# Kernel optimization log

Hardware: AMD Instinct MI355X
Metric: run time of the kernel (lower is better)

The kernel has to match this reference:

```python
import jax, jax.numpy as jnp
import numpy as np
from jax import lax

SIGMAS = [0.5, 1.0, 2.0, 4.0, 8.0]
FILTER_SIZE = int(4 * SIGMAS[-1] + 1)  # 33
PAD = int(2 * SIGMAS[-1])              # 16
DR = 1.0
C1 = (0.01 * DR) ** 2
C2 = (0.03 * DR) ** 2
ALPHA = 0.025
COMPENSATION = 200.0
LAMBDA_PIXEL = 100.0


def _gauss_2d(size, sigma):
    coords = np.arange(size, dtype=np.float32) - size // 2
    g = np.exp(-coords ** 2 / (2.0 * sigma ** 2))
    g = g / g.sum()
    return np.outer(g, g)  # (size, size)


def _build_g_masks():
    # Shape (15, 1, 33, 33): 3 identical copies per sigma, interleaved as in torch code.
    m = np.zeros((3 * len(SIGMAS), 1, FILTER_SIZE, FILTER_SIZE), dtype=np.float32)
    for idx, s in enumerate(SIGMAS):
        k = _gauss_2d(FILTER_SIZE, s)
        m[3 * idx + 0, 0] = k
        m[3 * idx + 1, 0] = k
        m[3 * idx + 2, 0] = k
    return jnp.asarray(m)


def _gconv(t, w):
    # Grouped conv, groups=3 (torch semantics: out channel j in group j // (O/3),
    # group g reads input channel g). 'same' padding via explicit PAD.
    return lax.conv_general_dilated(
        t, w, window_strides=(1, 1), padding=[(PAD, PAD), (PAD, PAD)],
        feature_group_count=3, dimension_numbers=('NCHW', 'OIHW', 'NCHW'))


def setup_inputs() -> dict:
    key = jax.random.key(0)
    k1, k2, k3 = jax.random.split(key, 3)
    x = jax.random.normal(k1, (8, 3, 512, 512), dtype=jnp.float32)
    y = jax.random.normal(k2, (8, 3, 512, 512), dtype=jnp.float32)
    disc_out = jax.random.normal(k3, (8, 1, 62, 62), dtype=jnp.float32)
    return {"x": x, "y": y, "disc_out": disc_out, "g_masks": _build_g_masks()}


def reference(x, y, disc_out, g_masks):
    # denormalize: tanh output [-1,1] -> [0,1]
    x = x * 0.5 + 0.5
    y = y * 0.5 + 0.5

    mux = _gconv(x, g_masks)          # (B, 15, H, W)
    muy = _gconv(y, g_masks)
    mux2 = mux * mux
    muy2 = muy * muy
    muxy = mux * muy
    sigmax2 = _gconv(x * x, g_masks) - mux2
    sigmay2 = _gconv(y * y, g_masks) - muy2
    sigmaxy = _gconv(x * y, g_masks) - muxy

    l = (2.0 * muxy + C1) / (mux2 + muy2 + C1)
    cs = (2.0 * sigmaxy + C2) / (sigmax2 + sigmay2 + C2)

    lM = l[:, -1] * l[:, -2] * l[:, -3]       # (B, H, W)
    PIcs = jnp.prod(cs, axis=1)               # (B, H, W)
    loss_ms_ssim = 1.0 - lM * PIcs

    loss_l1 = jnp.abs(x - y)                  # (B, 3, H, W)
    # narrow(0, -3, 3) -> last 3 filters (sigma=8), grouped conv then channel mean
    gaussian_l1 = _gconv(loss_l1, g_masks[-3:]).mean(axis=1)  # (B, H, W)

    loss_mix = ALPHA * loss_ms_ssim + (1.0 - ALPHA) * gaussian_l1 / DR
    loss_mix = COMPENSATION * loss_mix

    # GeneratorLoss: lambda_pixel * L1(x, y) + MSE(disc_out, 1)
    gen_loss = LAMBDA_PIXEL * jnp.mean(jnp.abs(x - y)) + jnp.mean((disc_out - 1.0) ** 2)

    return (loss_mix.mean() + gen_loss) / 2.0
```

## Files before the change

### kernel.cpp

```cpp
#include <hip/hip_runtime.h>
#include <stdint.h>


#define TILE 32
#define HALO 16
#define SSTR 72
#define PTPLN (32 * SSTR)
#define NT   256

#define C1c 1.0e-4f
#define C2c 9.0e-4f

typedef short bf16x8 __attribute__((ext_vector_type(8)));
typedef float f32x4  __attribute__((ext_vector_type(4)));
typedef unsigned short ush;

constexpr double cexp(double xx) {
  if (xx < -700.0) return 0.0;
  const double ln2 = 0.6931471805599453, il2 = 1.4426950408889634;
  double kd = xx * il2;
  long long k = (long long)(kd + (kd >= 0 ? 0.5 : -0.5));
  double r = xx - (double)k * ln2;
  double t = 1.0, s = 1.0;
  for (int i = 1; i <= 22; ++i) { t *= r / (double)i; s += t; }
  double p = 1.0, base = (k >= 0) ? 2.0 : 0.5;
  long long n = (k >= 0) ? k : -k;
  while (n) { if (n & 1) p *= base; base *= base; n >>= 1; }
  return s * p;
}
constexpr float gsi(double sigma) {
  double inv = 1.0 / (2.0 * sigma * sigma);
  double s = 0.0;
  for (int k = -16; k <= 16; ++k) s += cexp(-(double)(k * k) * inv);
  return (float)(1.0 / s);
}
constexpr float SI05 = gsi(0.5), SI10 = gsi(1.0), SI20 = gsi(2.0),
                SI40 = gsi(4.0), SI80 = gsi(8.0);

__device__ __forceinline__ unsigned f2bf_pk(float lo, float hi) {
  union { float f; unsigned u; } a, b; a.f = lo; b.f = hi;
  return __builtin_amdgcn_perm(b.u + 0x8000u, a.u + 0x8000u, 0x07060302u);
}
__device__ __forceinline__ ush f2bf1(float f) {
  union { float f; unsigned u; } c; c.f = f;
  return (ush)((c.u + 0x8000u) >> 16);
}

struct WFrag {
  bf16x8 h[2][2];
};

template<int SIG>
__device__ __forceinline__ void build_wm(ush* __restrict__ WM,
                                         const float (*__restrict__ wf5)[40],
                                         int tid, int wave, int lane,
                                         WFrag& W) {
  __syncthreads();
  #pragma unroll
  for (int i = 0; i < 8; ++i) {
    const int idx = i * 256 + tid;
    const int m = idx >> 6, k = idx & 63;
    const int t = k - m;
    const int tc = t < 0 ? 0 : (t > 32 ? 32 : t);
    float v = wf5[SIG][tc];
    v = (t >= 0 && t <= 32) ? v : 0.f;
    WM[m * SSTR + k] = f2bf1(v);
  }
  __syncthreads();
  const int l16 = lane & 15, quad = lane >> 4;
  #pragma unroll
  for (int t = 0; t < 2; ++t)
    #pragma unroll
    for (int c = 0; c < 2; ++c)
      W.h[t][c] = *(const bf16x8*)(WM + (t * 16 + l16) * SSTR + quad * 8 + 32 * c);
}

template<int NQ>
__device__ __forceinline__ void conv_pass(const bf16x8 (&A)[NQ][2],
                                          const WFrag& W,
                                          ush* __restrict__ PT,
                                          int wave, int lane, f32x4* V) {
  const int l16 = lane & 15, quad = lane >> 4;
  const int m0 = wave * 16;
  #pragma unroll
  for (int q = 0; q < NQ; ++q) {
    #pragma unroll
    for (int nt = 0; nt < 2; ++nt) {
      f32x4 acc = {0.f, 0.f, 0.f, 0.f};
      acc = __builtin_amdgcn_mfma_f32_16x16x32_bf16(A[q][0], W.h[nt][0], acc, 0, 0, 0);
      acc = __builtin_amdgcn_mfma_f32_16x16x32_bf16(A[q][1], W.h[nt][1], acc, 0, 0, 0);
      uint2 u;
      u.x = f2bf_pk(acc[0], acc[1]);
      u.y = f2bf_pk(acc[2], acc[3]);
      *(uint2*)(PT + q * PTPLN + (nt * 16 + l16) * SSTR + m0 + quad * 4) = u;
    }
  }
  const bf16x8 wv0 = (wave & 2) ? W.h[1][0] : W.h[0][0];
  const bf16x8 wv1 = (wave & 2) ? W.h[1][1] : W.h[0][1];
  __syncthreads();
  const int n0 = (wave & 1) * 16;
  #pragma unroll
  for (int q = 0; q < NQ; ++q) {
    const ush* pp = PT + q * PTPLN + (n0 + l16) * SSTR + quad * 8;
    const bf16x8 b0 = *(const bf16x8*)pp;
    const bf16x8 b1 = *(const bf16x8*)(pp + 32);
    f32x4 acc = {0.f, 0.f, 0.f, 0.f};
    acc = __builtin_amdgcn_mfma_f32_16x16x32_bf16(wv0, b0, acc, 0, 0, 0);
    acc = __builtin_amdgcn_mfma_f32_16x16x32_bf16(wv1, b1, acc, 0, 0, 0);
    V[q] = acc;
  }
}

__device__ __forceinline__ void ssim_fold(const f32x4* V, int mult, bool last,
                                          float* PIcs) {
  #pragma unroll
  for (int r = 0; r < 4; ++r) {
    const float mux = V[0][r], muy = V[1][r];
    const float A = mux * muy;
    const float Bq = mux * mux + muy * muy;
    const float S = V[2][r] + V[3][r] - Bq;
    const float sxy = V[4][r] - A;
    const float cs = (2.f * sxy + C2c) * __builtin_amdgcn_rcpf(S + C2c);
    float p = cs;
    if (mult >= 2) p *= cs;
    if (mult >= 3) p *= cs;
    if (last) {
      const float l = (2.f * A + C1c) * __builtin_amdgcn_rcpf(Bq + C1c);
      p *= l * l * l;
    }
    PIcs[r] *= p;
  }
}

__global__ __launch_bounds__(NT)
void msssim_fused_kernel(const float* __restrict__ x, const float* __restrict__ y,
                         const float* __restrict__ disc,
                         float* __restrict__ partials) {
  __shared__ ush PT[5 * PTPLN];
  __shared__ ush WM[32 * SSTR];
  __shared__ float wf5[5][40];
  __shared__ float red[12];

  const int tid = threadIdx.x;
  const int wave = tid >> 6, lane = tid & 63;
  const int l16 = lane & 15, quad = lane >> 4;
  const int bx = blockIdx.x, by = blockIdx.y, b = blockIdx.z;
  const int x0 = bx * TILE - HALO, y0 = by * TILE - HALO;
  const int blk = (b * 16 + by) * 16 + bx;

  const int gy = y0 + wave * 16 + l16;
  const int cbase = x0 + quad * 8;
  const bool rowok = (gy >= 0) && (gy < 512);

  float d2 = 0.f;
  { const int di = blk * 16 + tid;
    if (tid < 16 && di < 8 * 62 * 62) { const float dd = disc[di] - 1.f; d2 = dd * dd; } }

  if (tid < 165) {
    const int sig = tid / 33;
    const int k = tid - sig * 33;
    const float d = (float)(k - 16);
    float inv, si;
    if (sig == 0)      { inv = 2.0f;       si = SI05; }
    else if (sig == 1) { inv = 0.5f;       si = SI10; }
    else if (sig == 2) { inv = 0.125f;     si = SI20; }
    else if (sig == 3) { inv = 0.03125f;   si = SI40; }
    else               { inv = 0.0078125f; si = SI80; }
    wf5[sig][k] = __expf(-d * d * inv) * si;
  }

  float xr[16], yr[16];
  auto frag_loads = [&](int ch) {
    const float* __restrict__ xs = x + (size_t)(b * 3 + ch) * 262144;
    const float* __restrict__ ys = y + (size_t)(b * 3 + ch) * 262144;
    #pragma unroll
    for (int c = 0; c < 2; ++c) {
      const int g0 = cbase + 32 * c;
      if (rowok && g0 >= 0 && g0 <= 504) {
        const float* px = xs + gy * 512 + g0;
        const float* py = ys + gy * 512 + g0;
        const float4 a0 = *(const float4*)px;
        const float4 a1 = *(const float4*)(px + 4);
        const float4 b0 = *(const float4*)py;
        const float4 b1 = *(const float4*)(py + 4);
        xr[c*8+0]=a0.x; xr[c*8+1]=a0.y; xr[c*8+2]=a0.z; xr[c*8+3]=a0.w;
        xr[c*8+4]=a1.x; xr[c*8+5]=a1.y; xr[c*8+6]=a1.z; xr[c*8+7]=a1.w;
        yr[c*8+0]=b0.x; yr[c*8+1]=b0.y; yr[c*8+2]=b0.z; yr[c*8+3]=b0.w;
        yr[c*8+4]=b1.x; yr[c*8+5]=b1.y; yr[c*8+6]=b1.z; yr[c*8+7]=b1.w;
      } else {
        #pragma unroll
        for (int e = 0; e < 8; ++e) {
          const int g = g0 + e;
          const bool ok = rowok && (g >= 0) && (g < 512);
          xr[c*8+e] = ok ? xs[gy * 512 + g] : 0.f;
          yr[c*8+e] = ok ? ys[gy * 512 + g] : 0.f;
        }
      }
    }
  };

  float PIcs[4] = {1.f, 1.f, 1.f, 1.f};
  float sadf[16];
  #pragma unroll
  for (int e = 0; e < 16; ++e) sadf[e] = 0.f;

  f32x4 V[5];
  WFrag W;
  bf16x8 AF[5][2];

  auto derive = [&]() {
    #pragma unroll
    for (int c = 0; c < 2; ++c) {
      float xf[8], yf[8];
      #pragma unroll
      for (int e = 0; e < 8; ++e) {
        xf[e] = fmaf(xr[c*8+e], 0.5f, 0.5f);
        yf[e] = fmaf(yr[c*8+e], 0.5f, 0.5f);
        sadf[c*8+e] += fabsf(xf[e] - yf[e]);
      }
      union { unsigned u[4]; bf16x8 v; } w0, w1, w2, w3, w4;
      #pragma unroll
      for (int p = 0; p < 4; ++p) {
        w0.u[p] = f2bf_pk(xf[2*p],           xf[2*p+1]);
        w1.u[p] = f2bf_pk(yf[2*p],           yf[2*p+1]);
        w2.u[p] = f2bf_pk(xf[2*p]*xf[2*p],   xf[2*p+1]*xf[2*p+1]);
        w3.u[p] = f2bf_pk(yf[2*p]*yf[2*p],   yf[2*p+1]*yf[2*p+1]);
        w4.u[p] = f2bf_pk(xf[2*p]*yf[2*p],   xf[2*p+1]*yf[2*p+1]);
      }
      AF[0][c] = w0.v; AF[1][c] = w1.v; AF[2][c] = w2.v;
      AF[3][c] = w3.v; AF[4][c] = w4.v;
    }
  };

  frag_loads(0);
  derive();
  frag_loads(1);
  build_wm<0>(WM, wf5, tid, wave, lane, W);
  conv_pass<5>(AF, W, PT, wave, lane, V);
  ssim_fold(V, 3, false, PIcs);
  build_wm<1>(WM, wf5, tid, wave, lane, W);
  conv_pass<5>(AF, W, PT, wave, lane, V);
  ssim_fold(V, 2, false, PIcs);

  derive();
  frag_loads(2);
  __syncthreads();
  conv_pass<5>(AF, W, PT, wave, lane, V);
  ssim_fold(V, 1, false, PIcs);
  build_wm<2>(WM, wf5, tid, wave, lane, W);
  conv_pass<5>(AF, W, PT, wave, lane, V);
  ssim_fold(V, 3, false, PIcs);
  build_wm<3>(WM, wf5, tid, wave, lane, W);
  conv_pass<5>(AF, W, PT, wave, lane, V);
  ssim_fold(V, 1, false, PIcs);

  derive();
  __syncthreads();
  conv_pass<5>(AF, W, PT, wave, lane, V);
  ssim_fold(V, 2, false, PIcs);
  build_wm<4>(WM, wf5, tid, wave, lane, W);
  conv_pass<5>(AF, W, PT, wave, lane, V);
  ssim_fold(V, 3, true, PIcs);

  bf16x8 SF[1][2];
  #pragma unroll
  for (int c = 0; c < 2; ++c) {
    union { unsigned u[4]; bf16x8 v; } w;
    #pragma unroll
    for (int p = 0; p < 4; ++p)
      w.u[p] = f2bf_pk(sadf[c*8+2*p], sadf[c*8+2*p+1]);
    SF[0][c] = w.v;
  }
  __syncthreads();
  f32x4 V1[1];
  conv_pass<1>(SF, W, PT, wave, lane, V1);

  float absacc = 0.f;
  if (wave == 1 || wave == 2) {
    if (quad >= 2) {
      #pragma unroll
      for (int e = 0; e < 8; ++e) absacc += sadf[e];
    } else {
      #pragma unroll
      for (int e = 0; e < 8; ++e) absacc += sadf[8 + e];
    }
  }

  float mixsum = 0.f;
  #pragma unroll
  for (int r = 0; r < 4; ++r) {
    const float ssim = 1.f - PIcs[r];
    mixsum += 200.f * (0.025f * ssim + 0.975f * (V1[0][r] * (1.f / 3.f)));
  }

  #pragma unroll
  for (int off = 32; off > 0; off >>= 1) {
    mixsum += __shfl_down(mixsum, off);
    absacc += __shfl_down(absacc, off);
    d2     += __shfl_down(d2, off);
  }
  if (lane == 0) { red[wave] = mixsum; red[4 + wave] = absacc; red[8 + wave] = d2; }
  __syncthreads();
  if (tid == 0) {
    float m = 0.f, a = 0.f, d = 0.f;
    #pragma unroll
    for (int i = 0; i < 4; ++i) { m += red[i]; a += red[4 + i]; d += red[8 + i]; }
    partials[3 * blk + 0] = m;
    partials[3 * blk + 1] = a;
    partials[3 * blk + 2] = d;
  }
}

__global__ __launch_bounds__(512)
void msssim_final_kernel(const float* __restrict__ partials,
                         float* __restrict__ out) {
  __shared__ float red[24];
  const int tid = threadIdx.x;
  float m = 0.f, a = 0.f, d2 = 0.f;
  for (int j = tid; j < 2048; j += 512) {
    m  += partials[3 * j + 0];
    a  += partials[3 * j + 1];
    d2 += partials[3 * j + 2];
  }
  #pragma unroll
  for (int off = 32; off > 0; off >>= 1) {
    m  += __shfl_down(m, off);
    a  += __shfl_down(a, off);
    d2 += __shfl_down(d2, off);
  }
  const int wave = tid >> 6, lane = tid & 63;
  if (lane == 0) { red[wave] = m; red[8 + wave] = a; red[16 + wave] = d2; }
  __syncthreads();
  if (tid == 0) {
    float sm = 0.f, sa = 0.f, sd = 0.f;
    #pragma unroll
    for (int i = 0; i < 8; ++i) { sm += red[i]; sa += red[8 + i]; sd += red[16 + i]; }
    const float mix_mean  = sm / (8.f * 512.f * 512.f);
    const float abs_mean  = sa / (8.f * 3.f * 512.f * 512.f);
    const float disc_mean = sd / (8.f * 62.f * 62.f);
    out[0] = 0.5f * (mix_mean + 100.f * abs_mean + disc_mean);
  }
}

extern "C" void kernel_launch(void* const* d_in, const int* in_sizes, int n_in,
                              void* d_out, int out_size, void* d_ws, size_t ws_size,
                              hipStream_t stream) {
  const float* x    = (const float*)d_in[0];
  const float* y    = (const float*)d_in[1];
  const float* disc = (const float*)d_in[2];
  float* partials = (float*)d_ws;
  dim3 grid(16, 16, 8);
  msssim_fused_kernel<<<grid, NT, 0, stream>>>(x, y, disc, partials);
  msssim_final_kernel<<<1, 512, 0, stream>>>(partials, (float*)d_out);
}
```

Before: 144.2 us.

## Prebuild all sigma weight matrices and batch two conv passes per barrier

```diff
diff --git a/kernel.cpp b/kernel.cpp
--- a/kernel.cpp
+++ b/kernel.cpp
@@ -6,6 +6,7 @@
 #define HALO 16
 #define SSTR 72
 #define PTPLN (32 * SSTR)
+#define WMSZ  (32 * SSTR)
 #define NT   256
 
 #define C1c 1.0e-4f
@@ -50,36 +51,10 @@
   bf16x8 h[2][2];
 };
 
-template<int SIG>
-__device__ __forceinline__ void build_wm(ush* __restrict__ WM,
-                                         const float (*__restrict__ wf5)[40],
-                                         int tid, int wave, int lane,
-                                         WFrag& W) {
-  __syncthreads();
-  #pragma unroll
-  for (int i = 0; i < 8; ++i) {
-    const int idx = i * 256 + tid;
-    const int m = idx >> 6, k = idx & 63;
-    const int t = k - m;
-    const int tc = t < 0 ? 0 : (t > 32 ? 32 : t);
-    float v = wf5[SIG][tc];
-    v = (t >= 0 && t <= 32) ? v : 0.f;
-    WM[m * SSTR + k] = f2bf1(v);
-  }
-  __syncthreads();
-  const int l16 = lane & 15, quad = lane >> 4;
-  #pragma unroll
-  for (int t = 0; t < 2; ++t)
-    #pragma unroll
-    for (int c = 0; c < 2; ++c)
-      W.h[t][c] = *(const bf16x8*)(WM + (t * 16 + l16) * SSTR + quad * 8 + 32 * c);
-}
-
 template<int NQ>
-__device__ __forceinline__ void conv_pass(const bf16x8 (&A)[NQ][2],
-                                          const WFrag& W,
-                                          ush* __restrict__ PT,
-                                          int wave, int lane, f32x4* V) {
+__device__ __forceinline__ void conv_h(const bf16x8 (&A)[NQ][2], const WFrag& W,
+                                       ush* __restrict__ PT, int bp,
+                                       int wave, int lane) {
   const int l16 = lane & 15, quad = lane >> 4;
   const int m0 = wave * 16;
   #pragma unroll
@@ -92,16 +67,21 @@
       uint2 u;
       u.x = f2bf_pk(acc[0], acc[1]);
       u.y = f2bf_pk(acc[2], acc[3]);
-      *(uint2*)(PT + q * PTPLN + (nt * 16 + l16) * SSTR + m0 + quad * 4) = u;
-    }
-  }
+      *(uint2*)(PT + (bp + q) * PTPLN + (nt * 16 + l16) * SSTR + m0 + quad * 4) = u;
+    }
+  }
+}
+
+template<int NQ>
+__device__ __forceinline__ void conv_v(const WFrag& W, const ush* __restrict__ PT,
+                                       int bp, int wave, int lane, f32x4* V) {
+  const int l16 = lane & 15, quad = lane >> 4;
   const bf16x8 wv0 = (wave & 2) ? W.h[1][0] : W.h[0][0];
   const bf16x8 wv1 = (wave & 2) ? W.h[1][1] : W.h[0][1];
-  __syncthreads();
   const int n0 = (wave & 1) * 16;
   #pragma unroll
   for (int q = 0; q < NQ; ++q) {
-    const ush* pp = PT + q * PTPLN + (n0 + l16) * SSTR + quad * 8;
+    const ush* pp = PT + (bp + q) * PTPLN + (n0 + l16) * SSTR + quad * 8;
     const bf16x8 b0 = *(const bf16x8*)pp;
     const bf16x8 b1 = *(const bf16x8*)(pp + 32);
     f32x4 acc = {0.f, 0.f, 0.f, 0.f};
@@ -136,8 +116,8 @@
 void msssim_fused_kernel(const float* __restrict__ x, const float* __restrict__ y,
                          const float* __restrict__ disc,
                          float* __restrict__ partials) {
-  __shared__ ush PT[5 * PTPLN];
-  __shared__ ush WM[32 * SSTR];
+  __shared__ ush PT[11 * PTPLN];
+  __shared__ ush WM5[5 * WMSZ];
   __shared__ float wf5[5][40];
   __shared__ float red[12];
 
@@ -205,7 +185,6 @@
   for (int e = 0; e < 16; ++e) sadf[e] = 0.f;
 
   f32x4 V[5];
-  WFrag W;
   bf16x8 AF[5][2];
 
   auto derive = [&]() {
@@ -232,36 +211,60 @@
     }
   };
 
+  auto load_wfrag = [&](int sig, WFrag& W) {
+    const ush* base = WM5 + sig * WMSZ;
+    #pragma unroll
+    for (int t = 0; t < 2; ++t)
+      #pragma unroll
+      for (int c = 0; c < 2; ++c)
+        W.h[t][c] = *(const bf16x8*)(base + (t * 16 + l16) * SSTR + quad * 8 + 32 * c);
+  };
+
   frag_loads(0);
   derive();
   frag_loads(1);
-  build_wm<0>(WM, wf5, tid, wave, lane, W);
-  conv_pass<5>(AF, W, PT, wave, lane, V);
-  ssim_fold(V, 3, false, PIcs);
-  build_wm<1>(WM, wf5, tid, wave, lane, W);
-  conv_pass<5>(AF, W, PT, wave, lane, V);
-  ssim_fold(V, 2, false, PIcs);
-
+  __syncthreads();
+  #pragma unroll
+  for (int i = 0; i < 40; ++i) {
+    const int idx = i * 256 + tid;
+    const int sig = idx >> 11;
+    const int rem = idx & 2047;
+    const int m = rem >> 6, k = rem & 63;
+    const int t = k - m;
+    const int tc = t < 0 ? 0 : (t > 32 ? 32 : t);
+    float v = wf5[sig][tc];
+    v = (t >= 0 && t <= 32) ? v : 0.f;
+    WM5[sig * WMSZ + m * SSTR + k] = f2bf1(v);
+  }
+  __syncthreads();
+
+  WFrag WA, WB;
+  load_wfrag(0, WA);
+  load_wfrag(1, WB);
+
+  conv_h<5>(AF, WA, PT, 0, wave, lane);
+  conv_h<5>(AF, WB, PT, 5, wave, lane);
+  __syncthreads();
+  conv_v<5>(WA, PT, 0, wave, lane, V); ssim_fold(V, 3, false, PIcs);
+  conv_v<5>(WB, PT, 5, wave, lane, V); ssim_fold(V, 2, false, PIcs);
   derive();
   frag_loads(2);
-  __syncthreads();
-  conv_pass<5>(AF, W, PT, wave, lane, V);
-  ssim_fold(V, 1, false, PIcs);
-  build_wm<2>(WM, wf5, tid, wave, lane, W);
-  conv_pass<5>(AF, W, PT, wave, lane, V);
-  ssim_fold(V, 3, false, PIcs);
-  build_wm<3>(WM, wf5, tid, wave, lane, W);
-  conv_pass<5>(AF, W, PT, wave, lane, V);
-  ssim_fold(V, 1, false, PIcs);
-
+  load_wfrag(2, WA);
+  __syncthreads();
+
+  conv_h<5>(AF, WB, PT, 0, wave, lane);
+  conv_h<5>(AF, WA, PT, 5, wave, lane);
+  __syncthreads();
+  conv_v<5>(WB, PT, 0, wave, lane, V); ssim_fold(V, 1, false, PIcs);
+  conv_v<5>(WA, PT, 5, wave, lane, V); ssim_fold(V, 3, false, PIcs);
+  load_wfrag(3, WB);
+  __syncthreads();
+
+  conv_h<5>(AF, WB, PT, 0, wave, lane);
+  __syncthreads();
+  conv_v<5>(WB, PT, 0, wave, lane, V); ssim_fold(V, 1, false, PIcs);
   derive();
-  __syncthreads();
-  conv_pass<5>(AF, W, PT, wave, lane, V);
-  ssim_fold(V, 2, false, PIcs);
-  build_wm<4>(WM, wf5, tid, wave, lane, W);
-  conv_pass<5>(AF, W, PT, wave, lane, V);
-  ssim_fold(V, 3, true, PIcs);
-
+  load_wfrag(4, WA);
   bf16x8 SF[1][2];
   #pragma unroll
   for (int c = 0; c < 2; ++c) {
@@ -272,8 +275,15 @@
     SF[0][c] = w.v;
   }
   __syncthreads();
+
+  conv_h<5>(AF, WB, PT, 0, wave, lane);
+  conv_h<5>(AF, WA, PT, 5, wave, lane);
+  conv_h<1>(SF, WA, PT, 10, wave, lane);
+  __syncthreads();
+  conv_v<5>(WB, PT, 0, wave, lane, V); ssim_fold(V, 2, false, PIcs);
+  conv_v<5>(WA, PT, 5, wave, lane, V); ssim_fold(V, 3, true, PIcs);
   f32x4 V1[1];
-  conv_pass<1>(SF, W, PT, wave, lane, V1);
+  conv_v<1>(WA, PT, 10, wave, lane, V1);
 
   float absacc = 0.f;
   if (wave == 1 || wave == 2) {
```

New measurement: 141.8 us. Within noise of the previous version (-1.7%).
